# Kernel optimization log

Hardware: AMD Instinct MI355X
Metric: run time of the kernel (lower is better)

The kernel has to match this reference:

```python
import jax, jax.numpy as jnp
import numpy as np

B, S, D, E, H, K = 4, 2048, 1024, 8, 512, 2


def setup_inputs() -> dict:
    key = jax.random.key(0)
    ks = jax.random.split(key, 11)
    sc = 0.02
    return {
        "x": jax.random.normal(ks[0], (B, S, D), dtype=jnp.float32),
        "gate_W": jax.random.normal(ks[1], (D, E), dtype=jnp.float32) * sc,
        "W1": jax.random.normal(ks[2], (E, D, H), dtype=jnp.float32) * sc,
        "b1": jnp.zeros((E, H), dtype=jnp.float32),
        "W2": jax.random.normal(ks[3], (E, H, D), dtype=jnp.float32) * sc,
        "b2": jnp.zeros((E, D), dtype=jnp.float32),
        "Ws1": jax.random.normal(ks[4], (D, H), dtype=jnp.float32) * sc,
        "bs1": jnp.zeros((H,), dtype=jnp.float32),
        "Ws2": jax.random.normal(ks[5], (H, D), dtype=jnp.float32) * sc,
        "bs2": jnp.zeros((D,), dtype=jnp.float32),
        "route_scale": jnp.ones((), dtype=jnp.float32),
    }


def reference(x, gate_W, W1, b1, W2, b2, Ws1, bs1, Ws2, bs2, route_scale):
    # Gating: sigmoid scores scaled by route_scale (score_func='sigmoid')
    scores = jax.nn.sigmoid(x @ gate_W) * route_scale          # (B,S,E)
    topk_scores, topk_idx = jax.lax.top_k(scores, K)           # (B,S,K)
    topk_w = topk_scores / topk_scores.sum(-1, keepdims=True)  # normalized weights
    # Dense combine weights: zero for non-selected experts (same math as
    # the original sparse gather/scatter loop).
    onehot = jax.nn.one_hot(topk_idx, E, dtype=x.dtype)        # (B,S,K,E)
    gate_full = jnp.einsum('bsk,bske->bse', topk_w, onehot)    # (B,S,E)
    # Per-expert MLP applied to all tokens, combined with sparse gate weights.
    h = jax.nn.gelu(jnp.einsum('bsd,edh->bseh', x, W1) + b1, approximate=False)
    y = jnp.einsum('bseh,ehd->bsed', h, W2) + b2               # (B,S,E,D)
    expert_out = jnp.einsum('bse,bsed->bsd', gate_full, y)     # (B,S,D)
    # Shared expert MLP (always active)
    shared = jax.nn.gelu(x @ Ws1 + bs1, approximate=False) @ Ws2 + bs2
    return expert_out + shared
```

## Files before the change

kernel.cpp:

```cpp
#include <hip/hip_runtime.h>
#include <hip/hip_bf16.h>

#define TOKENS 8192
#define D_DIM  1024
#define E_NUM  8
#define H_DIM  512
#define N1     4608
#define CAP    3072
#define ET256  (CAP / 256)
#define EXP_ROWS (E_NUM * CAP)
#define SH_BASE  EXP_ROWS
#define HS_ROWS (EXP_ROWS + TOKENS)

typedef __bf16 bf16_t;
typedef __bf16 bf16x8 __attribute__((ext_vector_type(8)));
typedef __bf16 bf16x4 __attribute__((ext_vector_type(4)));
typedef float  f32x4  __attribute__((ext_vector_type(4)));

__device__ __forceinline__ float gelu_fast(float v) {
  float w = v * v;
  float t = __builtin_fmaf(w, 0.10294307f, 2.30258835f);
  float z = v * t;
  float e = __builtin_amdgcn_exp2f(z);
  float r = __builtin_amdgcn_rcpf(e + 1.0f);
  return v - v * r;
}

__global__ __launch_bounds__(256) void routing_kernel(
    const float* __restrict__ x, const float* __restrict__ gW,
    const float* __restrict__ route_scale, float* __restrict__ gateT,
    int* __restrict__ sel, bf16_t* __restrict__ Xb) {
  int tok  = blockIdx.x * 4 + (threadIdx.x >> 6);
  int lane = threadIdx.x & 63;
  const float* xr = x + (size_t)tok * D_DIM;
  double p[E_NUM];
#pragma unroll
  for (int e = 0; e < E_NUM; ++e) p[e] = 0.0;
  for (int d = lane; d < D_DIM; d += 64) {
    double xv = (double)xr[d];
    const float* g = gW + (size_t)d * E_NUM;
#pragma unroll
    for (int e = 0; e < E_NUM; ++e) p[e] += xv * (double)g[e];
  }
#pragma unroll
  for (int off = 32; off > 0; off >>= 1) {
#pragma unroll
    for (int e = 0; e < E_NUM; ++e) p[e] += __shfl_xor(p[e], off, 64);
  }
  if (lane == 0) {
    double rs = (double)route_scale[0];
    double s[E_NUM];
#pragma unroll
    for (int e = 0; e < E_NUM; ++e) s[e] = rs / (1.0 + exp(-p[e]));
    int i1 = 0;
#pragma unroll
    for (int e = 1; e < E_NUM; ++e) if (s[e] > s[i1]) i1 = e;
    int i2 = (i1 == 0) ? 1 : 0;
#pragma unroll
    for (int e = 0; e < E_NUM; ++e) if (e != i1 && s[e] > s[i2]) i2 = e;
    double inv = 1.0 / (s[i1] + s[i2]);
    float o[E_NUM];
#pragma unroll
    for (int e = 0; e < E_NUM; ++e) o[e] = 0.f;
    o[i1] = (float)(s[i1] * inv);
    o[i2] = (float)(s[i2] * inv);
#pragma unroll
    for (int e = 0; e < E_NUM; ++e) gateT[(size_t)e * TOKENS + tok] = o[e];
    sel[tok] = i1 * 8 + i2;
  }
  const float4* x4 = (const float4*)xr;
  bf16x4* xb4 = (bf16x4*)(Xb + (size_t)tok * D_DIM);
#pragma unroll
  for (int i = 0; i < 4; ++i) {
    float4 v = x4[i * 64 + lane];
    bf16x4 o = { (bf16_t)v.x, (bf16_t)v.y, (bf16_t)v.z, (bf16_t)v.w };
    xb4[i * 64 + lane] = o;
  }
}

__global__ __launch_bounds__(256) void repack1_kernel(
    const float* __restrict__ W1, const float* __restrict__ Ws1,
    bf16_t* __restrict__ Bt1) {
  __shared__ float tile[32][33];
  int k0 = blockIdx.x * 32, n0 = blockIdx.y * 32;
  int tx = threadIdx.x, ty = threadIdx.y;
#pragma unroll
  for (int i = 0; i < 4; ++i) {
    int kl = ty + i * 8;
    int n = n0 + tx, k = k0 + kl;
    float v;
    if (n0 < 4096) v = W1[(size_t)(n >> 9) * (D_DIM * H_DIM) + (size_t)k * H_DIM + (n & 511)];
    else           v = Ws1[(size_t)k * H_DIM + (n - 4096)];
    tile[kl][tx] = v;
  }
  __syncthreads();
#pragma unroll
  for (int i = 0; i < 4; ++i) {
    int nl = ty + i * 8;
    Bt1[(size_t)(n0 + nl) * D_DIM + k0 + tx] = (bf16_t)tile[tx][nl];
  }
}

__global__ __launch_bounds__(256) void repack2e_kernel(
    const float* __restrict__ W2, const float* __restrict__ Ws2,
    bf16_t* __restrict__ Bt2e) {
  __shared__ float tile[32][33];
  int d0 = blockIdx.x * 32, h0 = blockIdx.y * 32, e = blockIdx.z;
  int tx = threadIdx.x, ty = threadIdx.y;
#pragma unroll
  for (int i = 0; i < 4; ++i) {
    int hl = ty + i * 8;
    int h = h0 + hl, d = d0 + tx;
    float v = (e < E_NUM) ? W2[((size_t)e * H_DIM + h) * D_DIM + d]
                          : Ws2[(size_t)h * D_DIM + d];
    tile[hl][tx] = v;
  }
  __syncthreads();
#pragma unroll
  for (int i = 0; i < 4; ++i) {
    int dl = ty + i * 8;
    Bt2e[((size_t)e * D_DIM + (d0 + dl)) * H_DIM + h0 + tx] = (bf16_t)tile[tx][dl];
  }
}

__global__ __launch_bounds__(256) void listbuild_kernel(
    const float* __restrict__ gateT, const int* __restrict__ sel,
    int* __restrict__ perm, float* __restrict__ grow,
    int* __restrict__ tok2row, int* __restrict__ padcnt) {
  const int e = blockIdx.x;
  const int tid = threadIdx.x, lane = tid & 63, wid = tid >> 6;
  __shared__ int wsum[4];
  const float* row = gateT + (size_t)e * TOKENS;
  const int base = e * CAP;
  int running = 0;
  float gv = row[tid];
  for (int c = 0; c < TOKENS / 256; ++c) {
    float gv_next = (c + 1 < TOKENS / 256) ? row[(c + 1) * 256 + tid] : 0.f;
    const int tok = c * 256 + tid;
    const bool f = gv > 0.f;
    unsigned long long m = __ballot(f);
    int lanepre = __popcll(m & ((1ull << lane) - 1ull));
    if (lane == 0) wsum[wid] = __popcll(m);
    __syncthreads();
    int wbase = 0;
#pragma unroll
    for (int w2 = 0; w2 < 4; ++w2) if (w2 < wid) wbase += wsum[w2];
    const int tot = wsum[0] + wsum[1] + wsum[2] + wsum[3];
    if (f) {
      const int idx = running + wbase + lanepre;
      if (idx < CAP) {
        perm[base + idx] = tok;
        grow[base + idx] = gv;
        const int s = sel[tok];
        const int other = ((s >> 3) == e) ? (s & 7) : (s >> 3);
        tok2row[tok * 2 + (e > other ? 1 : 0)] = base + idx;
      }
    }
    running += tot;
    __syncthreads();
    gv = gv_next;
  }
  if (running > CAP) running = CAP;
  const int pc = (running + 255) & ~255;
  for (int i = running + tid; i < pc; i += 256) { perm[base + i] = 0; grow[base + i] = 0.f; }
  if (tid == 0) padcnt[e] = pc;
}

__device__ __forceinline__ void gemm_core256(
    const char* ga0, const char* ga1, const char* ga2, const char* ga3,
    const char* gb0, const char* gb1, const char* gb2, const char* gb3,
    int ktiles, char* lds, int wid, int lane, f32x4 (&acc)[8][4]) {
  const int wm = wid >> 2, wn = wid & 3;
  const int lA = lane & 15, kq = lane >> 4;
  const int slot0 = (kq ^ (lA & 7)) * 16;
  const int slot1 = ((4 + kq) ^ (lA & 7)) * 16;

  auto stage = [&](int buf, int t) {
    char* dA = lds + buf * 65536 + wid * 1024;
    char* dB = dA + 32768;
    const size_t ko = (size_t)t * 128;
    __builtin_amdgcn_global_load_lds((const __attribute__((address_space(1))) void*)(ga0 + ko),
        (__attribute__((address_space(3))) void*)(dA + 0 * 8192), 16, 0, 0);
    __builtin_amdgcn_global_load_lds((const __attribute__((address_space(1))) void*)(ga1 + ko),
        (__attribute__((address_space(3))) void*)(dA + 1 * 8192), 16, 0, 0);
    __builtin_amdgcn_global_load_lds((const __attribute__((address_space(1))) void*)(ga2 + ko),
        (__attribute__((address_space(3))) void*)(dA + 2 * 8192), 16, 0, 0);
    __builtin_amdgcn_global_load_lds((const __attribute__((address_space(1))) void*)(ga3 + ko),
        (__attribute__((address_space(3))) void*)(dA + 3 * 8192), 16, 0, 0);
    __builtin_amdgcn_global_load_lds((const __attribute__((address_space(1))) void*)(gb0 + ko),
        (__attribute__((address_space(3))) void*)(dB + 0 * 8192), 16, 0, 0);
    __builtin_amdgcn_global_load_lds((const __attribute__((address_space(1))) void*)(gb1 + ko),
        (__attribute__((address_space(3))) void*)(dB + 1 * 8192), 16, 0, 0);
    __builtin_amdgcn_global_load_lds((const __attribute__((address_space(1))) void*)(gb2 + ko),
        (__attribute__((address_space(3))) void*)(dB + 2 * 8192), 16, 0, 0);
    __builtin_amdgcn_global_load_lds((const __attribute__((address_space(1))) void*)(gb3 + ko),
        (__attribute__((address_space(3))) void*)(dB + 3 * 8192), 16, 0, 0);
  };

  stage(0, 0);
  for (int t = 0; t < ktiles; ++t) {
    const int b = t & 1;
    asm volatile("s_waitcnt vmcnt(0)" ::: "memory");
    __builtin_amdgcn_s_barrier();
    asm volatile("" ::: "memory");
    if (t + 1 < ktiles) stage(b ^ 1, t + 1);
    const char* Ab = lds + b * 65536 + wm * 16384;
    const char* Bb = lds + b * 65536 + 32768 + (wn >> 1) * 16384 + ((wn & 1) * 64) * 128;
    bf16x8 bfv[4][2];
#pragma unroll
    for (int nf = 0; nf < 4; ++nf) {
      const int rb = (nf * 16 + lA) * 128;
      bfv[nf][0] = *(const bf16x8*)(Bb + rb + slot0);
      bfv[nf][1] = *(const bf16x8*)(Bb + rb + slot1);
    }
#pragma unroll
    for (int qm = 0; qm < 2; ++qm) {
      bf16x8 af[4][2];
#pragma unroll
      for (int i = 0; i < 4; ++i) {
        const int ra = ((qm * 4 + i) * 16 + lA) * 128;
        af[i][0] = *(const bf16x8*)(Ab + ra + slot0);
        af[i][1] = *(const bf16x8*)(Ab + ra + slot1);
      }
      __builtin_amdgcn_s_setprio(1);
#pragma unroll
      for (int i = 0; i < 4; ++i)
#pragma unroll
        for (int nf = 0; nf < 4; ++nf) {
          acc[qm * 4 + i][nf] = __builtin_amdgcn_mfma_f32_16x16x32_bf16(af[i][0], bfv[nf][0], acc[qm * 4 + i][nf], 0, 0, 0);
          acc[qm * 4 + i][nf] = __builtin_amdgcn_mfma_f32_16x16x32_bf16(af[i][1], bfv[nf][1], acc[qm * 4 + i][nf], 0, 0, 0);
        }
      __builtin_amdgcn_s_setprio(0);
      __builtin_amdgcn_sched_barrier(0);
    }
  }
}

__device__ __forceinline__ int swz_src(int lane) {
  return ((lane & 7) ^ ((lane >> 3) & 7)) * 16;
}

__global__ __launch_bounds__(512, 2) void gemm1e_kernel(
    const bf16_t* __restrict__ Xb, const bf16_t* __restrict__ Bt1,
    const int* __restrict__ perm, const float* __restrict__ grow,
    const int* __restrict__ padcnt,
    const float* __restrict__ b1, const float* __restrict__ bs1,
    bf16_t* __restrict__ Hs) {
  __shared__ bf16_t sL[65536];
  const int t = threadIdx.x, wid = t >> 6, lane = t & 63;
  const int y = blockIdx.y;
  int e, rowbase;
  if (y < E_NUM * ET256) {
    e = y / ET256;
    const int lt = y - e * ET256;
    if (lt * 256 >= padcnt[e]) return;
    rowbase = e * CAP + lt * 256;
  } else {
    e = E_NUM;
    rowbase = SH_BASE + (y - E_NUM * ET256) * 256;
  }
  const int n0 = blockIdx.x * 256;
  const int rl = wid * 8 + (lane >> 3);
  const int sc = swz_src(lane);
  const char *ga[4], *gb[4];
#pragma unroll
  for (int g = 0; g < 4; ++g) {
    const int r = g * 64 + rl;
    const int tok = (e < E_NUM) ? perm[rowbase + r] : (rowbase - SH_BASE + r);
    ga[g] = (const char*)Xb + (size_t)tok * 2048 + sc;
    gb[g] = (const char*)(Bt1 + (size_t)e * H_DIM * D_DIM) + (size_t)(n0 + r) * 2048 + sc;
  }
  f32x4 acc[8][4];
#pragma unroll
  for (int i = 0; i < 8; ++i)
#pragma unroll
    for (int j = 0; j < 4; ++j) acc[i][j] = (f32x4){0.f, 0.f, 0.f, 0.f};
  gemm_core256(ga[0], ga[1], ga[2], ga[3], gb[0], gb[1], gb[2], gb[3],
               D_DIM / 64, (char*)sL, wid, lane, acc);

  const int wm = wid >> 2, wn = wid & 3, lA = lane & 15;
  const float* bias = (e < E_NUM) ? (b1 + e * H_DIM) : bs1;
#pragma unroll
  for (int mf = 0; mf < 8; ++mf) {
    const int rloc = wm * 128 + mf * 16 + (lane >> 4) * 4;
    float gr[4];
#pragma unroll
    for (int q = 0; q < 4; ++q)
      gr[q] = (e < E_NUM) ? grow[rowbase + rloc + q] : 1.0f;
#pragma unroll
    for (int nf = 0; nf < 4; ++nf) {
      const int col = n0 + wn * 64 + nf * 16 + lA;
      const float bv = bias[col];
#pragma unroll
      for (int q = 0; q < 4; ++q) {
        float v = gelu_fast(acc[mf][nf][q] + bv);
        Hs[(size_t)(rowbase + rloc + q) * H_DIM + col] = (bf16_t)(v * gr[q]);
      }
    }
  }
}

__global__ __launch_bounds__(512, 2) void gemm2e_kernel(
    const bf16_t* __restrict__ Hs, const bf16_t* __restrict__ Bt2e,
    const float* __restrict__ grow, const int* __restrict__ padcnt,
    const float* __restrict__ b2, bf16_t* __restrict__ Ys) {
  __shared__ bf16_t sL[65536];
  const int t = threadIdx.x, wid = t >> 6, lane = t & 63;
  const int y = blockIdx.y;
  const int e = y / ET256;
  const int lt = y - e * ET256;
  if (lt * 256 >= padcnt[e]) return;
  const int rowbase = e * CAP + lt * 256;
  const int n0 = blockIdx.x * 256;
  const int rl = wid * 8 + (lane >> 3);
  const int sc = swz_src(lane);
  const char *ga[4], *gb[4];
#pragma unroll
  for (int g = 0; g < 4; ++g) {
    const int r = g * 64 + rl;
    ga[g] = (const char*)Hs + (size_t)(rowbase + r) * 1024 + sc;
    gb[g] = (const char*)(Bt2e + (size_t)e * D_DIM * H_DIM) + (size_t)(n0 + r) * 1024 + sc;
  }
  f32x4 acc[8][4];
#pragma unroll
  for (int i = 0; i < 8; ++i)
#pragma unroll
    for (int j = 0; j < 4; ++j) acc[i][j] = (f32x4){0.f, 0.f, 0.f, 0.f};
  gemm_core256(ga[0], ga[1], ga[2], ga[3], gb[0], gb[1], gb[2], gb[3],
               H_DIM / 64, (char*)sL, wid, lane, acc);

  const int wm = wid >> 2, wn = wid & 3, lA = lane & 15;
  const float* bb = b2 + (size_t)e * D_DIM;
#pragma unroll
  for (int mf = 0; mf < 8; ++mf) {
    const int rloc = wm * 128 + mf * 16 + (lane >> 4) * 4;
    float gr[4];
#pragma unroll
    for (int q = 0; q < 4; ++q) gr[q] = grow[rowbase + rloc + q];
#pragma unroll
    for (int nf = 0; nf < 4; ++nf) {
      const int col = n0 + wn * 64 + nf * 16 + lA;
      const float bv = bb[col];
#pragma unroll
      for (int q = 0; q < 4; ++q)
        Ys[(size_t)(rowbase + rloc + q) * D_DIM + col] = (bf16_t)(acc[mf][nf][q] + gr[q] * bv);
    }
  }
}

__global__ __launch_bounds__(512, 2) void gemm2s_kernel(
    const bf16_t* __restrict__ Hs, const bf16_t* __restrict__ Bt2e,
    const int* __restrict__ tok2row, const float* __restrict__ bs2,
    const bf16_t* __restrict__ Ys, float* __restrict__ out) {
  __shared__ bf16_t sL[65536];
  const int t = threadIdx.x, wid = t >> 6, lane = t & 63;
  const int tokbase = blockIdx.y * 256;
  const int rowbase = SH_BASE + tokbase;
  const int n0 = blockIdx.x * 256;
  const int rl = wid * 8 + (lane >> 3);
  const int sc = swz_src(lane);
  const char *ga[4], *gb[4];
#pragma unroll
  for (int g = 0; g < 4; ++g) {
    const int r = g * 64 + rl;
    ga[g] = (const char*)Hs + (size_t)(rowbase + r) * 1024 + sc;
    gb[g] = (const char*)(Bt2e + (size_t)E_NUM * D_DIM * H_DIM) + (size_t)(n0 + r) * 1024 + sc;
  }
  f32x4 acc[8][4];
#pragma unroll
  for (int i = 0; i < 8; ++i)
#pragma unroll
    for (int j = 0; j < 4; ++j) acc[i][j] = (f32x4){0.f, 0.f, 0.f, 0.f};
  gemm_core256(ga[0], ga[1], ga[2], ga[3], gb[0], gb[1], gb[2], gb[3],
               H_DIM / 64, (char*)sL, wid, lane, acc);

  const int wm = wid >> 2, wn = wid & 3, lA = lane & 15;
#pragma unroll
  for (int mf = 0; mf < 8; ++mf) {
    const int rloc = wm * 128 + mf * 16 + (lane >> 4) * 4;
    int r0[4], r1[4];
#pragma unroll
    for (int q = 0; q < 4; ++q) {
      const int tok = tokbase + rloc + q;
      r0[q] = tok2row[tok * 2];
      r1[q] = tok2row[tok * 2 + 1];
    }
#pragma unroll
    for (int nf = 0; nf < 4; ++nf) {
      const int col = n0 + wn * 64 + nf * 16 + lA;
      const float bv = bs2[col];
#pragma unroll
      for (int q = 0; q < 4; ++q) {
        const int tok = tokbase + rloc + q;
        float y0 = (float)Ys[(size_t)r0[q] * D_DIM + col];
        float y1 = (float)Ys[(size_t)r1[q] * D_DIM + col];
        out[(size_t)tok * D_DIM + col] = acc[mf][nf][q] + bv + y0 + y1;
      }
    }
  }
}

extern "C" void kernel_launch(void* const* d_in, const int* in_sizes, int n_in,
                              void* d_out, int out_size, void* d_ws, size_t ws_size,
                              hipStream_t stream) {
  (void)in_sizes; (void)n_in; (void)out_size; (void)ws_size;
  const float* x    = (const float*)d_in[0];
  const float* gW   = (const float*)d_in[1];
  const float* W1   = (const float*)d_in[2];
  const float* b1   = (const float*)d_in[3];
  const float* W2   = (const float*)d_in[4];
  const float* b2   = (const float*)d_in[5];
  const float* Ws1  = (const float*)d_in[6];
  const float* bs1  = (const float*)d_in[7];
  const float* Ws2  = (const float*)d_in[8];
  const float* bs2  = (const float*)d_in[9];
  const float* rsc  = (const float*)d_in[10];
  float* out = (float*)d_out;

  char* w = (char*)d_ws;
  float*  gateT = (float*)w;  w += (size_t)E_NUM * TOKENS * 4;
  int*    sel   = (int*)w;    w += (size_t)TOKENS * 4;
  bf16_t* Xb    = (bf16_t*)w; w += (size_t)TOKENS * D_DIM * 2;
  bf16_t* Bt1   = (bf16_t*)w; w += (size_t)N1 * D_DIM * 2;
  bf16_t* Bt2e  = (bf16_t*)w; w += (size_t)9 * D_DIM * H_DIM * 2;
  bf16_t* Hs    = (bf16_t*)w; w += (size_t)HS_ROWS * H_DIM * 2;
  bf16_t* Ys    = (bf16_t*)w; w += (size_t)EXP_ROWS * D_DIM * 2;
  int*    perm  = (int*)w;    w += (size_t)EXP_ROWS * 4;
  float*  grow  = (float*)w;  w += (size_t)EXP_ROWS * 4;
  int*    tok2row = (int*)w;  w += (size_t)TOKENS * 2 * 4;
  int*    padcnt  = (int*)w;

  routing_kernel<<<TOKENS / 4, 256, 0, stream>>>(x, gW, rsc, gateT, sel, Xb);
  listbuild_kernel<<<E_NUM, 256, 0, stream>>>(gateT, sel, perm, grow, tok2row, padcnt);
  repack1_kernel<<<dim3(D_DIM / 32, N1 / 32), dim3(32, 8), 0, stream>>>(W1, Ws1, Bt1);
  repack2e_kernel<<<dim3(D_DIM / 32, H_DIM / 32, 9), dim3(32, 8), 0, stream>>>(W2, Ws2, Bt2e);

  gemm1e_kernel<<<dim3(H_DIM / 256, E_NUM * ET256 + TOKENS / 256), dim3(512), 0, stream>>>(
      Xb, Bt1, perm, grow, padcnt, b1, bs1, Hs);
  gemm2e_kernel<<<dim3(D_DIM / 256, E_NUM * ET256), dim3(512), 0, stream>>>(
      Hs, Bt2e, grow, padcnt, b2, Ys);
  gemm2s_kernel<<<dim3(D_DIM / 256, TOKENS / 256), dim3(512), 0, stream>>>(
      Hs, Bt2e, tok2row, bs2, Ys, out);
}
```

Measured before the change: 158.0 us.

## Restructure GEMM mainloop into barrier-synchronized quarter-tile ping-pong schedule

The K-loop of the shared 256-tile GEMM core is rewritten. It now processes two k-tiles per iteration with fixed buffer indices, and each tile is split into four quarter steps. Each step loads A fragments, issues the next tile's global-to-LDS prefetch in the first quarter, and brackets the MFMA bursts with s_barrier to keep the waves in lockstep. The aim is to interleave LDS reads, global prefetch and MFMA more finely so memory latency is hidden and the waves issue in a ping-pong pattern. It adds many more barriers per tile and assumes ktiles is even, since an odd count would drop the last tile.

After: 168.6 us. 6.7% more time.

```diff
diff --git a/kernel.cpp b/kernel.cpp
--- a/kernel.cpp
+++ b/kernel.cpp
@@ -166,6 +166,11 @@
   if (tid == 0) padcnt[e] = pc;
 }
 
+__device__ __forceinline__ void gload16(const char* src, char* dst) {
+  __builtin_amdgcn_global_load_lds((const __attribute__((address_space(1))) void*)src,
+      (__attribute__((address_space(3))) void*)dst, 16, 0, 0);
+}
+
 __device__ __forceinline__ void gemm_core256(
     const char* ga0, const char* ga1, const char* ga2, const char* ga3,
     const char* gb0, const char* gb1, const char* gb2, const char* gb3,
@@ -175,63 +180,68 @@
   const int slot0 = (kq ^ (lA & 7)) * 16;
   const int slot1 = ((4 + kq) ^ (lA & 7)) * 16;
 
-  auto stage = [&](int buf, int t) {
+  auto stage8 = [&](int buf, int t) {
     char* dA = lds + buf * 65536 + wid * 1024;
     char* dB = dA + 32768;
     const size_t ko = (size_t)t * 128;
-    __builtin_amdgcn_global_load_lds((const __attribute__((address_space(1))) void*)(ga0 + ko),
-        (__attribute__((address_space(3))) void*)(dA + 0 * 8192), 16, 0, 0);
-    __builtin_amdgcn_global_load_lds((const __attribute__((address_space(1))) void*)(ga1 + ko),
-        (__attribute__((address_space(3))) void*)(dA + 1 * 8192), 16, 0, 0);
-    __builtin_amdgcn_global_load_lds((const __attribute__((address_space(1))) void*)(ga2 + ko),
-        (__attribute__((address_space(3))) void*)(dA + 2 * 8192), 16, 0, 0);
-    __builtin_amdgcn_global_load_lds((const __attribute__((address_space(1))) void*)(ga3 + ko),
-        (__attribute__((address_space(3))) void*)(dA + 3 * 8192), 16, 0, 0);
-    __builtin_amdgcn_global_load_lds((const __attribute__((address_space(1))) void*)(gb0 + ko),
-        (__attribute__((address_space(3))) void*)(dB + 0 * 8192), 16, 0, 0);
-    __builtin_amdgcn_global_load_lds((const __attribute__((address_space(1))) void*)(gb1 + ko),
-        (__attribute__((address_space(3))) void*)(dB + 1 * 8192), 16, 0, 0);
-    __builtin_amdgcn_global_load_lds((const __attribute__((address_space(1))) void*)(gb2 + ko),
-        (__attribute__((address_space(3))) void*)(dB + 2 * 8192), 16, 0, 0);
-    __builtin_amdgcn_global_load_lds((const __attribute__((address_space(1))) void*)(gb3 + ko),
-        (__attribute__((address_space(3))) void*)(dB + 3 * 8192), 16, 0, 0);
+    gload16(ga0 + ko, dA + 0 * 8192);
+    gload16(ga1 + ko, dA + 1 * 8192);
+    gload16(ga2 + ko, dA + 2 * 8192);
+    gload16(ga3 + ko, dA + 3 * 8192);
+    gload16(gb0 + ko, dB + 0 * 8192);
+    gload16(gb1 + ko, dB + 1 * 8192);
+    gload16(gb2 + ko, dB + 2 * 8192);
+    gload16(gb3 + ko, dB + 3 * 8192);
   };
 
-  stage(0, 0);
-  for (int t = 0; t < ktiles; ++t) {
-    const int b = t & 1;
-    asm volatile("s_waitcnt vmcnt(0)" ::: "memory");
-    __builtin_amdgcn_s_barrier();
-    asm volatile("" ::: "memory");
-    if (t + 1 < ktiles) stage(b ^ 1, t + 1);
-    const char* Ab = lds + b * 65536 + wm * 16384;
-    const char* Bb = lds + b * 65536 + 32768 + (wn >> 1) * 16384 + ((wn & 1) * 64) * 128;
-    bf16x8 bfv[4][2];
-#pragma unroll
-    for (int nf = 0; nf < 4; ++nf) {
-      const int rb = (nf * 16 + lA) * 128;
-      bfv[nf][0] = *(const bf16x8*)(Bb + rb + slot0);
-      bfv[nf][1] = *(const bf16x8*)(Bb + rb + slot1);
-    }
-#pragma unroll
-    for (int qm = 0; qm < 2; ++qm) {
-      bf16x8 af[4][2];
-#pragma unroll
-      for (int i = 0; i < 4; ++i) {
-        const int ra = ((qm * 4 + i) * 16 + lA) * 128;
-        af[i][0] = *(const bf16x8*)(Ab + ra + slot0);
-        af[i][1] = *(const bf16x8*)(Ab + ra + slot1);
+  stage8(0, 0);
+  asm volatile("s_waitcnt vmcnt(0)" ::: "memory");
+  __builtin_amdgcn_s_barrier();
+
+  const int niter = ktiles >> 1;
+  for (int j = 0; j < niter; ++j) {
+#pragma unroll
+    for (int half = 0; half < 2; ++half) {
+      const int tcur = 2 * j + half;
+      const int bb = half;
+      const char* Ab = lds + bb * 65536 + wm * 16384;
+      const char* Bb = lds + bb * 65536 + 32768 + (wn >> 1) * 16384 + (wn & 1) * 64 * 128;
+      bf16x8 bfv[4][2];
+#pragma unroll
+      for (int q = 0; q < 4; ++q) {
+        bf16x8 af[2][2];
+#pragma unroll
+        for (int i = 0; i < 2; ++i) {
+          const char* ra = Ab + (size_t)((q * 2 + i) * 16 + lA) * 128;
+          af[i][0] = *(const bf16x8*)(ra + slot0);
+          af[i][1] = *(const bf16x8*)(ra + slot1);
+        }
+        if (q == 0) {
+#pragma unroll
+          for (int nf = 0; nf < 4; ++nf) {
+            const char* rb = Bb + (size_t)(nf * 16 + lA) * 128;
+            bfv[nf][0] = *(const bf16x8*)(rb + slot0);
+            bfv[nf][1] = *(const bf16x8*)(rb + slot1);
+          }
+          if (tcur + 1 < ktiles) stage8(bb ^ 1, tcur + 1);
+        }
+        asm volatile("" ::: "memory");
+        __builtin_amdgcn_s_barrier();
+        asm volatile("s_waitcnt lgkmcnt(0)" ::: "memory");
+        __builtin_amdgcn_sched_barrier(0);
+        __builtin_amdgcn_s_setprio(1);
+#pragma unroll
+        for (int i = 0; i < 2; ++i)
+#pragma unroll
+          for (int nf = 0; nf < 4; ++nf) {
+            acc[q * 2 + i][nf] = __builtin_amdgcn_mfma_f32_16x16x32_bf16(af[i][0], bfv[nf][0], acc[q * 2 + i][nf], 0, 0, 0);
+            acc[q * 2 + i][nf] = __builtin_amdgcn_mfma_f32_16x16x32_bf16(af[i][1], bfv[nf][1], acc[q * 2 + i][nf], 0, 0, 0);
+          }
+        __builtin_amdgcn_s_setprio(0);
+        if (q == 3) asm volatile("s_waitcnt vmcnt(0)" ::: "memory");
+        asm volatile("" ::: "memory");
+        __builtin_amdgcn_s_barrier();
       }
-      __builtin_amdgcn_s_setprio(1);
-#pragma unroll
-      for (int i = 0; i < 4; ++i)
-#pragma unroll
-        for (int nf = 0; nf < 4; ++nf) {
-          acc[qm * 4 + i][nf] = __builtin_amdgcn_mfma_f32_16x16x32_bf16(af[i][0], bfv[nf][0], acc[qm * 4 + i][nf], 0, 0, 0);
-          acc[qm * 4 + i][nf] = __builtin_amdgcn_mfma_f32_16x16x32_bf16(af[i][1], bfv[nf][1], acc[qm * 4 + i][nf], 0, 0, 0);
-        }
-      __builtin_amdgcn_s_setprio(0);
-      __builtin_amdgcn_sched_barrier(0);
     }
   }
 }
```

## Issue next-tile prefetch before waiting and remap blocks for XCD-aware locality

Applied to the files above, without the earlier changes.

The GEMM core now issues the next K-tile's global-to-LDS loads before waiting on the current tile, using vmcnt(8) so the prefetch stays in flight. A trailing barrier is added so the buffer is not overwritten while other waves still read it. Separately, the three GEMM kernels remap linear block IDs so blocks that land on the same XCD (round-robin by ID mod 8) share B columns and row tiles, aiming for better L2 reuse. The extra barrier per iteration adds synchronisation cost.

New measurement: 167.3 us. +5.9%, slower.

```diff
diff --git a/kernel.cpp b/kernel.cpp
--- a/kernel.cpp
+++ b/kernel.cpp
@@ -166,6 +166,11 @@
   if (tid == 0) padcnt[e] = pc;
 }
 
+__device__ __forceinline__ void gload16(const char* src, char* dst) {
+  __builtin_amdgcn_global_load_lds((const __attribute__((address_space(1))) void*)src,
+      (__attribute__((address_space(3))) void*)dst, 16, 0, 0);
+}
+
 __device__ __forceinline__ void gemm_core256(
     const char* ga0, const char* ga1, const char* ga2, const char* ga3,
     const char* gb0, const char* gb1, const char* gb2, const char* gb3,
@@ -175,35 +180,31 @@
   const int slot0 = (kq ^ (lA & 7)) * 16;
   const int slot1 = ((4 + kq) ^ (lA & 7)) * 16;
 
-  auto stage = [&](int buf, int t) {
+  auto stage8 = [&](int buf, int t) {
     char* dA = lds + buf * 65536 + wid * 1024;
     char* dB = dA + 32768;
     const size_t ko = (size_t)t * 128;
-    __builtin_amdgcn_global_load_lds((const __attribute__((address_space(1))) void*)(ga0 + ko),
-        (__attribute__((address_space(3))) void*)(dA + 0 * 8192), 16, 0, 0);
-    __builtin_amdgcn_global_load_lds((const __attribute__((address_space(1))) void*)(ga1 + ko),
-        (__attribute__((address_space(3))) void*)(dA + 1 * 8192), 16, 0, 0);
-    __builtin_amdgcn_global_load_lds((const __attribute__((address_space(1))) void*)(ga2 + ko),
-        (__attribute__((address_space(3))) void*)(dA + 2 * 8192), 16, 0, 0);
-    __builtin_amdgcn_global_load_lds((const __attribute__((address_space(1))) void*)(ga3 + ko),
-        (__attribute__((address_space(3))) void*)(dA + 3 * 8192), 16, 0, 0);
-    __builtin_amdgcn_global_load_lds((const __attribute__((address_space(1))) void*)(gb0 + ko),
-        (__attribute__((address_space(3))) void*)(dB + 0 * 8192), 16, 0, 0);
-    __builtin_amdgcn_global_load_lds((const __attribute__((address_space(1))) void*)(gb1 + ko),
-        (__attribute__((address_space(3))) void*)(dB + 1 * 8192), 16, 0, 0);
-    __builtin_amdgcn_global_load_lds((const __attribute__((address_space(1))) void*)(gb2 + ko),
-        (__attribute__((address_space(3))) void*)(dB + 2 * 8192), 16, 0, 0);
-    __builtin_amdgcn_global_load_lds((const __attribute__((address_space(1))) void*)(gb3 + ko),
-        (__attribute__((address_space(3))) void*)(dB + 3 * 8192), 16, 0, 0);
+    gload16(ga0 + ko, dA + 0 * 8192);
+    gload16(ga1 + ko, dA + 1 * 8192);
+    gload16(ga2 + ko, dA + 2 * 8192);
+    gload16(ga3 + ko, dA + 3 * 8192);
+    gload16(gb0 + ko, dB + 0 * 8192);
+    gload16(gb1 + ko, dB + 1 * 8192);
+    gload16(gb2 + ko, dB + 2 * 8192);
+    gload16(gb3 + ko, dB + 3 * 8192);
   };
 
-  stage(0, 0);
+  stage8(0, 0);
   for (int t = 0; t < ktiles; ++t) {
     const int b = t & 1;
-    asm volatile("s_waitcnt vmcnt(0)" ::: "memory");
+    if (t + 1 < ktiles) {
+      stage8(b ^ 1, t + 1);
+      asm volatile("s_waitcnt vmcnt(8)" ::: "memory");
+    } else {
+      asm volatile("s_waitcnt vmcnt(0)" ::: "memory");
+    }
     __builtin_amdgcn_s_barrier();
     asm volatile("" ::: "memory");
-    if (t + 1 < ktiles) stage(b ^ 1, t + 1);
     const char* Ab = lds + b * 65536 + wm * 16384;
     const char* Bb = lds + b * 65536 + 32768 + (wn >> 1) * 16384 + ((wn & 1) * 64) * 128;
     bf16x8 bfv[4][2];
@@ -233,6 +234,8 @@
       __builtin_amdgcn_s_setprio(0);
       __builtin_amdgcn_sched_barrier(0);
     }
+    asm volatile("" ::: "memory");
+    __builtin_amdgcn_s_barrier();
   }
 }
 
@@ -248,18 +251,21 @@
     bf16_t* __restrict__ Hs) {
   __shared__ bf16_t sL[65536];
   const int t = threadIdx.x, wid = t >> 6, lane = t & 63;
-  const int y = blockIdx.y;
+  const int L = blockIdx.x + 2 * blockIdx.y;
+  const int xc = L & 7, ii = L >> 3;
+  const int bx = xc >> 2;
+  const int by = (xc & 3) * 32 + ii;
   int e, rowbase;
-  if (y < E_NUM * ET256) {
-    e = y / ET256;
-    const int lt = y - e * ET256;
+  if (by < E_NUM * ET256) {
+    e = by / ET256;
+    const int lt = by - e * ET256;
     if (lt * 256 >= padcnt[e]) return;
     rowbase = e * CAP + lt * 256;
   } else {
     e = E_NUM;
-    rowbase = SH_BASE + (y - E_NUM * ET256) * 256;
-  }
-  const int n0 = blockIdx.x * 256;
+    rowbase = SH_BASE + (by - E_NUM * ET256) * 256;
+  }
+  const int n0 = bx * 256;
   const int rl = wid * 8 + (lane >> 3);
   const int sc = swz_src(lane);
   const char *ga[4], *gb[4];
@@ -306,12 +312,15 @@
     const float* __restrict__ b2, bf16_t* __restrict__ Ys) {
   __shared__ bf16_t sL[65536];
   const int t = threadIdx.x, wid = t >> 6, lane = t & 63;
-  const int y = blockIdx.y;
-  const int e = y / ET256;
-  const int lt = y - e * ET256;
+  const int L = blockIdx.x + 4 * blockIdx.y;
+  const int xc = L & 7, ii = L >> 3;
+  const int bx = xc >> 1;
+  const int by = (xc & 1) * 48 + ii;
+  const int e = by / ET256;
+  const int lt = by - e * ET256;
   if (lt * 256 >= padcnt[e]) return;
   const int rowbase = e * CAP + lt * 256;
-  const int n0 = blockIdx.x * 256;
+  const int n0 = bx * 256;
   const int rl = wid * 8 + (lane >> 3);
   const int sc = swz_src(lane);
   const char *ga[4], *gb[4];
@@ -354,9 +363,13 @@
     const bf16_t* __restrict__ Ys, float* __restrict__ out) {
   __shared__ bf16_t sL[65536];
   const int t = threadIdx.x, wid = t >> 6, lane = t & 63;
-  const int tokbase = blockIdx.y * 256;
+  const int L = blockIdx.x + 4 * blockIdx.y;
+  const int xc = L & 7, ii = L >> 3;
+  const int bx = xc >> 1;
+  const int by = (xc & 1) * 16 + ii;
+  const int tokbase = by * 256;
   const int rowbase = SH_BASE + tokbase;
-  const int n0 = blockIdx.x * 256;
+  const int n0 = bx * 256;
   const int rl = wid * 8 + (lane >> 3);
   const int sc = swz_src(lane);
   const char *ga[4], *gb[4];
```
